# Optimization experiments

Hardware: AMD Instinct MI355X
Metric: run time of the kernel (lower is better)

Reference implementation:

```python
import jax, jax.numpy as jnp
import numpy as np

N, M, D, H = 2048, 32, 768, 512
TEMP, THRESH, EPS = 0.05, 1e-4, 1e-6


def setup_inputs() -> dict:
    key = jax.random.key(0)
    ks = jax.random.split(key, 7)
    q = jax.random.normal(ks[0], (D,), dtype=jnp.float32)
    X = jax.random.normal(ks[1], (N, D), dtype=jnp.float32)
    C_init = jax.random.normal(ks[2], (M, D), dtype=jnp.float32)
    # nn.Linear default init: U(-1/sqrt(fan_in), 1/sqrt(fan_in))
    s1 = 1.0 / np.sqrt(5 * D)
    W1 = jax.random.uniform(ks[3], (5 * D, H), jnp.float32, -s1, s1)
    b1 = jax.random.uniform(ks[4], (H,), jnp.float32, -s1, s1)
    s2 = 1.0 / np.sqrt(H)
    W2 = jax.random.uniform(ks[5], (H, 1), jnp.float32, -s2, s2)
    b2 = jax.random.uniform(ks[6], (1,), jnp.float32, -s2, s2)
    return {"q": q, "X": X, "C_init": C_init, "W1": W1, "b1": b1, "W2": W2, "b2": b2}


def _learned_dist(q, x, y, W1, b1, W2, b2):
    # pairwise features: for each (i,j): [x_i, y_j, |x_i-y_j|, |x_i-q|, |y_j-q|]
    n, m, d = x.shape[0], y.shape[0], x.shape[1]
    xb = jnp.broadcast_to(x[:, None, :], (n, m, d))
    yb = jnp.broadcast_to(y[None, :, :], (n, m, d))
    feat = jnp.concatenate(
        [xb, yb, jnp.abs(xb - yb), jnp.abs(xb - q), jnp.abs(yb - q)], axis=-1
    )  # (n, m, 5d)
    h = jax.nn.relu(jnp.einsum("nmf,fh->nmh", feat, W1) + b1)
    return jax.nn.sigmoid(jnp.einsum("nmh,ho->nmo", h, W2)[..., 0] + b2[0])  # (n, m)


def reference(q, X, C_init, W1, b1, W2, b2):
    d = -_learned_dist(q, X, C_init, W1, b1, W2, b2)          # (N, M)
    a = jax.nn.softmax(d / TEMP, axis=1)                       # (N, M)
    a_sum = jnp.sum(a, axis=0) + EPS                           # (M,)
    C_new = (a.T @ X) / a_sum[:, None]                         # (M, D)
    # Torch loop always recomputes with C_init, so it runs at most once and
    # returns C_new iff the initial diff exceeds the threshold, else C_init.
    diff = jnp.sum(jnp.abs(C_new - C_init))                    # L1 norm
    C_final = jnp.where(diff > THRESH, C_new, C_init)
    return (C_final, a)
```

## Files before the change

kernel.cpp:

```cpp
#include <hip/hip_runtime.h>
#include <hip/hip_fp16.h>
#include <math.h>

#define NN 2048
#define MM 32
#define DD 768
#define HH 512
#define KT 24
#define WBLK ((size_t)KT * 16384)
constexpr float TEMP = 0.05f;
constexpr float THRESH = 1e-4f;
constexpr float EPS = 1e-6f;

typedef _Float16 halfx8 __attribute__((ext_vector_type(8)));
typedef float floatx4 __attribute__((ext_vector_type(4)));

__device__ __forceinline__ halfx8 habs8(halfx8 a, halfx8 b) {
    halfx8 d = a - b;
    union { halfx8 h; unsigned int u[4]; } x;
    x.h = d;
    #pragma unroll
    for (int e = 0; e < 4; ++e) x.u[e] &= 0x7FFF7FFFu;
    return x.h;
}

__global__ __launch_bounds__(256) void prep_kernel(
    const float* __restrict__ X, const float* __restrict__ W1,
    _Float16* __restrict__ Xf, _Float16* __restrict__ Wf)
{
    __shared__ float Wt[32 * 512];
    const int t = threadIdx.x;
    if (blockIdx.x < 192) {
        #pragma unroll
        for (int p = 0; p < 4; ++p) {
            int u = blockIdx.x * 1024 + p * 256 + t;
            int it = u / 1536;
            int rem = u - it * 1536;
            int kt = rem >> 6;
            int lane = rem & 63;
            int row = it * 16 + (lane & 15);
            int kb = kt * 32 + (lane >> 4) * 8;
            const float* xp = X + (size_t)row * DD + kb;
            float4 xa = *(const float4*)xp;
            float4 xb = *(const float4*)(xp + 4);
            halfx8 v;
            v[0] = (_Float16)xa.x; v[1] = (_Float16)xa.y;
            v[2] = (_Float16)xa.z; v[3] = (_Float16)xa.w;
            v[4] = (_Float16)xb.x; v[5] = (_Float16)xb.y;
            v[6] = (_Float16)xb.z; v[7] = (_Float16)xb.w;
            *(halfx8*)(Xf + (size_t)u * 8) = v;
        }
    } else {
        const int b = blockIdx.x - 192;
        const int wb = b / 24;
        const int kt = b % 24;
        const int rowbase = wb * 768;
        #pragma unroll
        for (int rep = 0; rep < 16; ++rep) {
            int idx = rep * 256 + t;
            int row = idx >> 7;
            int c4 = (idx & 127) * 4;
            *(float4*)&Wt[row * 512 + c4] =
                *(const float4*)(W1 + (size_t)(rowbase + kt * 32 + row) * HH + c4);
        }
        __syncthreads();
        #pragma unroll
        for (int g = 0; g < 8; ++g) {
            halfx8 v;
            #pragma unroll
            for (int jj = 0; jj < 8; ++jj) {
                int o = t * 64 + g * 8 + jj;
                int nt = o >> 9;
                int l  = (o >> 3) & 63;
                int j  = o & 7;
                int k  = ((l >> 4) << 3) + j;
                int n  = nt * 16 + (l & 15);
                v[jj] = (_Float16)Wt[k * 512 + n];
            }
            *(halfx8*)(Wf + (size_t)wb * WBLK + (size_t)kt * 16384 + t * 64 + g * 8) = v;
        }
    }
}

__global__ __launch_bounds__(512, 2) void build_AB_kernel(
    const float* __restrict__ q, const float* __restrict__ C_init,
    const _Float16* __restrict__ Xf, const _Float16* __restrict__ Wf,
    const float* __restrict__ b1,
    _Float16* __restrict__ Arowh, float* __restrict__ Brow)
{
    __shared__ __align__(16) char smem[67584];
    const int t = threadIdx.x;
    const int lane = t & 63;
    const int wv = t >> 6;
    const int q4 = lane >> 4;
    const int l16 = lane & 15;

    if (blockIdx.x < 256) {
        _Float16* qh = (_Float16*)smem;
        const int hs = blockIdx.x & 3;
        const int by = blockIdx.x >> 2;
        const int nt = hs * 8 + wv;

        for (int d = t; d < DD; d += 512) qh[d] = (_Float16)q[d];
        __syncthreads();

        const _Float16* ap0 = Xf + ((size_t)((by * 2 + 0) * 24) * 64 + lane) * 8;
        const _Float16* ap1 = Xf + ((size_t)((by * 2 + 1) * 24) * 64 + lane) * 8;
        const _Float16* bpA = Wf + (size_t)nt * 512 + (size_t)lane * 8;
        const _Float16* bpD = Wf + 3 * WBLK + (size_t)nt * 512 + (size_t)lane * 8;

        floatx4 acc[2];
        acc[0] = (floatx4)0.f; acc[1] = (floatx4)0.f;

        halfx8 Afc[2], Bac, Bdc, Afn[2], Ban, Bdn;
        Afc[0] = *(const halfx8*)ap0;
        Afc[1] = *(const halfx8*)ap1;
        Bac = *(const halfx8*)bpA;
        Bdc = *(const halfx8*)bpD;

        for (int kt = 0; kt < KT; ++kt) {
            if (kt < KT - 1) {
                Afn[0] = *(const halfx8*)(ap0 + (kt + 1) * 512);
                Afn[1] = *(const halfx8*)(ap1 + (kt + 1) * 512);
                Ban = *(const halfx8*)(bpA + (size_t)(kt + 1) * 16384);
                Bdn = *(const halfx8*)(bpD + (size_t)(kt + 1) * 16384);
            }
            halfx8 qf = *(halfx8*)&qh[kt * 32 + q4 * 8];
            #pragma unroll
            for (int rt = 0; rt < 2; ++rt) {
                halfx8 Zd = habs8(Afc[rt], qf);
                acc[rt] = __builtin_amdgcn_mfma_f32_16x16x32_f16(Afc[rt], Bac, acc[rt], 0, 0, 0);
                acc[rt] = __builtin_amdgcn_mfma_f32_16x16x32_f16(Zd, Bdc, acc[rt], 0, 0, 0);
            }
            Afc[0] = Afn[0]; Afc[1] = Afn[1]; Bac = Ban; Bdc = Bdn;
        }
        #pragma unroll
        for (int rt = 0; rt < 2; ++rt)
            #pragma unroll
            for (int reg = 0; reg < 4; ++reg) {
                int i = by * 32 + rt * 16 + q4 * 4 + reg;
                int h = nt * 16 + l16;
                Arowh[(size_t)i * HH + h] = (_Float16)acc[rt][reg];
            }
    } else {
        _Float16* yh = (_Float16*)smem;
        _Float16* qh = yh + 32 * 776;
        floatx4* Bred = (floatx4*)(smem + (32 * 776 + DD) * 2);
        const int nt = blockIdx.x - 256;

        for (int r = 0; r < 32; ++r)
            for (int d = t; d < DD; d += 512)
                yh[r * 776 + d] = (_Float16)C_init[(size_t)r * DD + d];
        for (int d = t; d < DD; d += 512) qh[d] = (_Float16)q[d];
        __syncthreads();

        const _Float16* Wb = Wf + 1 * WBLK;
        const _Float16* We = Wf + 4 * WBLK;

        floatx4 acc[2];
        acc[0] = (floatx4)0.f; acc[1] = (floatx4)0.f;

        #pragma unroll
        for (int r = 0; r < 3; ++r) {
            int kt = wv + r * 8;
            halfx8 qf = *(halfx8*)&qh[kt * 32 + q4 * 8];
            size_t wo = (size_t)kt * 16384 + (size_t)nt * 512 + (size_t)lane * 8;
            halfx8 Bb = *(const halfx8*)(Wb + wo);
            halfx8 Be = *(const halfx8*)(We + wo);
            #pragma unroll
            for (int rt = 0; rt < 2; ++rt) {
                halfx8 Ab = *(halfx8*)&yh[(rt * 16 + l16) * 776 + kt * 32 + q4 * 8];
                halfx8 Ze = habs8(Ab, qf);
                acc[rt] = __builtin_amdgcn_mfma_f32_16x16x32_f16(Ab, Bb, acc[rt], 0, 0, 0);
                acc[rt] = __builtin_amdgcn_mfma_f32_16x16x32_f16(Ze, Be, acc[rt], 0, 0, 0);
            }
        }
        Bred[(wv * 2 + 0) * 64 + lane] = acc[0];
        Bred[(wv * 2 + 1) * 64 + lane] = acc[1];
        __syncthreads();
        if (wv < 2) {
            int rt = wv;
            floatx4 s = Bred[rt * 64 + lane];
            #pragma unroll
            for (int w = 1; w < 8; ++w) s += Bred[(w * 2 + rt) * 64 + lane];
            #pragma unroll
            for (int reg = 0; reg < 4; ++reg) {
                int j = rt * 16 + q4 * 4 + reg;
                int h = nt * 16 + l16;
                Brow[(size_t)j * HH + h] = s[reg] + b1[h];
            }
        }
    }
}

__global__ __launch_bounds__(512, 4) void pairwise_kernel(
    const _Float16* __restrict__ Xf, const _Float16* __restrict__ Wf,
    const float* __restrict__ Y,
    const _Float16* __restrict__ Arowh, const float* __restrict__ Brow,
    const float* __restrict__ W2, float* __restrict__ Spart)
{
    __shared__ _Float16 yh[2 * DD];
    __shared__ float Sred[2][4][64];
    const int t = threadIdx.x;
    const int lane = t & 63;
    const int wv = t >> 6;
    const int wr = wv >> 2;
    const int cq = wv & 3;
    const int q4 = lane >> 4;
    const int l16 = lane & 15;
    const int i0 = blockIdx.x * 64;
    const int hs = blockIdx.y & 1;
    const int j0 = (blockIdx.y >> 1) * 2;

    for (int d = t; d < DD; d += 512) {
        yh[d]      = (_Float16)Y[(size_t)j0 * DD + d];
        yh[DD + d] = (_Float16)Y[(size_t)(j0 + 1) * DD + d];
    }
    __syncthreads();

    const _Float16* Wc = Wf + 2 * WBLK;
    const _Float16* ap0 = Xf + ((size_t)((blockIdx.x * 4 + wr * 2 + 0) * 24) * 64 + lane) * 8;
    const _Float16* ap1 = Xf + ((size_t)((blockIdx.x * 4 + wr * 2 + 1) * 24) * 64 + lane) * 8;
    const _Float16* bp = Wc + (size_t)(hs * 16 + cq * 4) * 512 + (size_t)lane * 8;

    floatx4 acc[2][2][4];
    #pragma unroll
    for (int jj = 0; jj < 2; ++jj)
        #pragma unroll
        for (int rt = 0; rt < 2; ++rt)
            #pragma unroll
            for (int ct = 0; ct < 4; ++ct) acc[jj][rt][ct] = (floatx4)0.f;

    for (int kt = 0; kt < KT; ++kt) {
        halfx8 Af[2], Bf[4], hv[2];
        Af[0] = *(const halfx8*)(ap0 + kt * 512);
        Af[1] = *(const halfx8*)(ap1 + kt * 512);
        #pragma unroll
        for (int ct = 0; ct < 4; ++ct)
            Bf[ct] = *(const halfx8*)(bp + (size_t)kt * 16384 + ct * 512);
        hv[0] = *(halfx8*)&yh[kt * 32 + q4 * 8];
        hv[1] = *(halfx8*)&yh[DD + kt * 32 + q4 * 8];
        #pragma unroll
        for (int jj = 0; jj < 2; ++jj)
            #pragma unroll
            for (int rt = 0; rt < 2; ++rt) {
                halfx8 Zf = habs8(Af[rt], hv[jj]);
                #pragma unroll
                for (int ct = 0; ct < 4; ++ct)
                    acc[jj][rt][ct] = __builtin_amdgcn_mfma_f32_16x16x32_f16(
                        Zf, Bf[ct], acc[jj][rt][ct], 0, 0, 0);
            }
    }

    float w2v[4], bv[2][4];
    #pragma unroll
    for (int ct = 0; ct < 4; ++ct) {
        int h = hs * 256 + cq * 64 + ct * 16 + l16;
        w2v[ct] = W2[h];
        bv[0][ct] = Brow[(size_t)j0 * HH + h];
        bv[1][ct] = Brow[(size_t)(j0 + 1) * HH + h];
    }
    #pragma unroll
    for (int rt = 0; rt < 2; ++rt)
        #pragma unroll
        for (int reg = 0; reg < 4; ++reg) {
            int row = wr * 32 + rt * 16 + q4 * 4 + reg;
            const _Float16* ap = Arowh + (size_t)(i0 + row) * HH + hs * 256 + cq * 64 + l16;
            float av[4];
            #pragma unroll
            for (int ct = 0; ct < 4; ++ct) av[ct] = (float)ap[ct * 16];
            #pragma unroll
            for (int jj = 0; jj < 2; ++jj) {
                float s = 0.f;
                #pragma unroll
                for (int ct = 0; ct < 4; ++ct) {
                    float pre = acc[jj][rt][ct][reg] + av[ct] + bv[jj][ct];
                    s = fmaf(fmaxf(pre, 0.f), w2v[ct], s);
                }
                s += __shfl_xor(s, 1, 64);
                s += __shfl_xor(s, 2, 64);
                s += __shfl_xor(s, 4, 64);
                s += __shfl_xor(s, 8, 64);
                if (l16 == 0) Sred[jj][cq][row] = s;
            }
        }
    __syncthreads();
    if (t < 128) {
        int row = t & 63, jj = t >> 6;
        float s = Sred[jj][0][row] + Sred[jj][1][row] + Sred[jj][2][row] + Sred[jj][3][row];
        Spart[((size_t)hs * NN + (i0 + row)) * MM + j0 + jj] = s;
    }
}

__global__ __launch_bounds__(256) void cnew_sm_kernel(
    const float* __restrict__ Spart, const float* __restrict__ b2,
    const float* __restrict__ X,
    float* __restrict__ a_out, float* __restrict__ Cpart,
    float* __restrict__ Apart)
{
    __shared__ float a_s[64][36];
    const int t = threadIdx.x;
    const int dc = blockIdx.x;
    const int ic = blockIdx.y;
    const int ibase = ic * 64;
    const float b2v = b2[0];

    {
        const int j = t & 31, r = t >> 5;
        #pragma unroll
        for (int rb = 0; rb < 8; ++rb) {
            int il = rb * 8 + r;
            int i = ibase + il;
            float s = Spart[(size_t)i * MM + j] + Spart[(size_t)(NN + i) * MM + j];
            float sig = 1.f / (1.f + expf(-(s + b2v)));
            float l = -sig * (1.0f / TEMP);
            float m = l;
            #pragma unroll
            for (int off = 16; off >= 1; off >>= 1) m = fmaxf(m, __shfl_xor(m, off, 32));
            float e = expf(l - m);
            float sum = e;
            #pragma unroll
            for (int off = 16; off >= 1; off >>= 1) sum += __shfl_xor(sum, off, 32);
            a_s[il][j] = e / sum;
        }
    }
    __syncthreads();
    if (dc == 0) {
        #pragma unroll
        for (int p = 0; p < 8; ++p) {
            int k = p * 256 + t;
            a_out[(size_t)(ibase + (k >> 5)) * MM + (k & 31)] = a_s[k >> 5][k & 31];
        }
    }
    const int dl = t & 63, jg = t >> 6;
    const int d = dc * 64 + dl;
    float acc[8] = {};
    float asum[8] = {};
    #pragma unroll 4
    for (int ii = 0; ii < 64; ++ii) {
        float xv = X[(size_t)(ibase + ii) * DD + d];
        float4 a0 = *(float4*)&a_s[ii][jg * 8];
        float4 a1 = *(float4*)&a_s[ii][jg * 8 + 4];
        acc[0] = fmaf(a0.x, xv, acc[0]); asum[0] += a0.x;
        acc[1] = fmaf(a0.y, xv, acc[1]); asum[1] += a0.y;
        acc[2] = fmaf(a0.z, xv, acc[2]); asum[2] += a0.z;
        acc[3] = fmaf(a0.w, xv, acc[3]); asum[3] += a0.w;
        acc[4] = fmaf(a1.x, xv, acc[4]); asum[4] += a1.x;
        acc[5] = fmaf(a1.y, xv, acc[5]); asum[5] += a1.y;
        acc[6] = fmaf(a1.z, xv, acc[6]); asum[6] += a1.z;
        acc[7] = fmaf(a1.w, xv, acc[7]); asum[7] += a1.w;
    }
    #pragma unroll
    for (int jj = 0; jj < 8; ++jj)
        Cpart[((size_t)ic * MM + jg * 8 + jj) * DD + d] = acc[jj];
    if (dc == 0 && dl == 0)
        #pragma unroll
        for (int jj = 0; jj < 8; ++jj)
            Apart[ic * MM + jg * 8 + jj] = asum[jj];
}

__global__ __launch_bounds__(256) void merge_kernel(
    const float* __restrict__ Cpart, const float* __restrict__ Apart,
    const float* __restrict__ C_init, float* __restrict__ C_new,
    float* __restrict__ Dpart)
{
    __shared__ float wred[4];
    const int dc = blockIdx.x;
    const int j = blockIdx.y;
    const int t = threadIdx.x;
    const int d = dc * 256 + t;
    float asum = 0.f;
    #pragma unroll
    for (int ic = 0; ic < 32; ++ic) asum += Apart[ic * MM + j];
    const float inv = 1.f / (asum + EPS);
    float s = 0.f;
    #pragma unroll
    for (int ic = 0; ic < 32; ++ic)
        s += Cpart[((size_t)ic * MM + j) * DD + d];
    float c = s * inv;
    C_new[(size_t)j * DD + d] = c;
    float ad = fabsf(c - C_init[(size_t)j * DD + d]);
    #pragma unroll
    for (int off = 32; off >= 1; off >>= 1) ad += __shfl_xor(ad, off, 64);
    if ((t & 63) == 0) wred[t >> 6] = ad;
    __syncthreads();
    if (t == 0) Dpart[j * 3 + dc] = wred[0] + wred[1] + wred[2] + wred[3];
}

__global__ __launch_bounds__(256) void select_kernel(
    const float* __restrict__ C_new, const float* __restrict__ C_init,
    const float* __restrict__ Dpart, float* __restrict__ out)
{
    __shared__ float ds[96];
    const int t = threadIdx.x;
    if (t < 96) ds[t] = Dpart[t];
    __syncthreads();
    float dv = 0.f;
    #pragma unroll
    for (int p = 0; p < 96; ++p) dv += ds[p];
    const int k = blockIdx.x * 256 + t;
    out[k] = (dv > THRESH) ? C_new[k] : C_init[k];
}

extern "C" void kernel_launch(void* const* d_in, const int* in_sizes, int n_in,
                              void* d_out, int out_size, void* d_ws, size_t ws_size,
                              hipStream_t stream)
{
    const float* q      = (const float*)d_in[0];
    const float* X      = (const float*)d_in[1];
    const float* C_init = (const float*)d_in[2];
    const float* W1     = (const float*)d_in[3];
    const float* b1     = (const float*)d_in[4];
    const float* W2     = (const float*)d_in[5];
    const float* b2     = (const float*)d_in[6];

    float* out_C = (float*)d_out;
    float* out_a = (float*)d_out + (size_t)MM * DD;

    float* ws = (float*)d_ws;
    _Float16* Wf    = (_Float16*)ws;
    _Float16* Xf    = (_Float16*)(ws + 983040);
    _Float16* Arowh = (_Float16*)(ws + 1769472);
    float* Brow  = ws + 2293760;
    float* Spart = ws + 2310144;
    float* Cpart = ws + 2441216;
    float* Apart = ws + 3227648;
    float* Dpart = ws + 3228672;
    float* Cn    = ws + 3228768;

    prep_kernel<<<312, 256, 0, stream>>>(X, W1, Xf, Wf);
    build_AB_kernel<<<288, 512, 0, stream>>>(q, C_init, Xf, Wf, b1, Arowh, Brow);
    pairwise_kernel<<<dim3(32, 32), 512, 0, stream>>>(Xf, Wf, C_init, Arowh, Brow, W2, Spart);
    cnew_sm_kernel<<<dim3(12, 32), 256, 0, stream>>>(Spart, b2, X, out_a, Cpart, Apart);
    merge_kernel<<<dim3(3, 32), 256, 0, stream>>>(Cpart, Apart, C_init, Cn, Dpart);
    select_kernel<<<96, 256, 0, stream>>>(Cn, C_init, Dpart, out_C);
}
```

Before: 182.7 us.

## Retile pairwise kernel to one centroid per block with async LDS-staged X

Each pairwise block now handles a single centroid j across the full hidden dimension, with each wave owning a 64-wide hidden slice and all 64 rows. X fragments are staged into shared memory through double-buffered global_load_lds, so one X chunk is reused by all eight waves instead of each wave loading its own from global memory. This removes the two-way hidden split and its partial-sum buffer, so the softmax kernel reads one S value per entry. In exchange each wave holds more accumulators, the kernel uses more LDS, and W1 reuse across two centroids per block is lost, which may hurt occupancy and raise weight traffic.

```diff
diff --git a/kernel.cpp b/kernel.cpp
--- a/kernel.cpp
+++ b/kernel.cpp
@@ -197,103 +197,110 @@
     const _Float16* __restrict__ Xf, const _Float16* __restrict__ Wf,
     const float* __restrict__ Y,
     const _Float16* __restrict__ Arowh, const float* __restrict__ Brow,
-    const float* __restrict__ W2, float* __restrict__ Spart)
-{
-    __shared__ _Float16 yh[2 * DD];
-    __shared__ float Sred[2][4][64];
+    const float* __restrict__ W2, float* __restrict__ S)
+{
+    __shared__ _Float16 XfL[2 * 24 * 512];
+    __shared__ _Float16 yh[DD];
+    __shared__ float Sred[8][64];
     const int t = threadIdx.x;
     const int lane = t & 63;
     const int wv = t >> 6;
-    const int wr = wv >> 2;
-    const int cq = wv & 3;
     const int q4 = lane >> 4;
     const int l16 = lane & 15;
     const int i0 = blockIdx.x * 64;
-    const int hs = blockIdx.y & 1;
-    const int j0 = (blockIdx.y >> 1) * 2;
-
-    for (int d = t; d < DD; d += 512) {
-        yh[d]      = (_Float16)Y[(size_t)j0 * DD + d];
-        yh[DD + d] = (_Float16)Y[(size_t)(j0 + 1) * DD + d];
-    }
+    const int j  = blockIdx.y;
+
+    for (int d = t; d < DD; d += 512) yh[d] = (_Float16)Y[(size_t)j * DD + d];
+
+    const _Float16* Wc = Wf + 2 * WBLK;
+    const _Float16* bp = Wc + (size_t)(wv * 4) * 512 + (size_t)lane * 8;
+
+    auto stage = [&](int c, int buf) {
+        #pragma unroll
+        for (int s = 0; s < 3; ++s) {
+            int p = wv * 3 + s;
+            int ktc = p >> 2, it = p & 3;
+            const _Float16* src = Xf
+                + ((size_t)((blockIdx.x * 4 + it) * 24 + c * 6 + ktc) * 64 + lane) * 8;
+            _Float16* dst = &XfL[(buf * 24 + p) * 512];
+            __builtin_amdgcn_global_load_lds(
+                (const __attribute__((address_space(1))) unsigned int*)(const void*)src,
+                (__attribute__((address_space(3))) unsigned int*)(void*)dst, 16, 0, 0);
+        }
+    };
+
+    floatx4 acc[4][4];
+    #pragma unroll
+    for (int rt = 0; rt < 4; ++rt)
+        #pragma unroll
+        for (int ct = 0; ct < 4; ++ct) acc[rt][ct] = (floatx4)0.f;
+
+    stage(0, 0);
     __syncthreads();
 
-    const _Float16* Wc = Wf + 2 * WBLK;
-    const _Float16* ap0 = Xf + ((size_t)((blockIdx.x * 4 + wr * 2 + 0) * 24) * 64 + lane) * 8;
-    const _Float16* ap1 = Xf + ((size_t)((blockIdx.x * 4 + wr * 2 + 1) * 24) * 64 + lane) * 8;
-    const _Float16* bp = Wc + (size_t)(hs * 16 + cq * 4) * 512 + (size_t)lane * 8;
-
-    floatx4 acc[2][2][4];
-    #pragma unroll
-    for (int jj = 0; jj < 2; ++jj)
-        #pragma unroll
-        for (int rt = 0; rt < 2; ++rt)
-            #pragma unroll
-            for (int ct = 0; ct < 4; ++ct) acc[jj][rt][ct] = (floatx4)0.f;
-
-    for (int kt = 0; kt < KT; ++kt) {
-        halfx8 Af[2], Bf[4], hv[2];
-        Af[0] = *(const halfx8*)(ap0 + kt * 512);
-        Af[1] = *(const halfx8*)(ap1 + kt * 512);
-        #pragma unroll
-        for (int ct = 0; ct < 4; ++ct)
-            Bf[ct] = *(const halfx8*)(bp + (size_t)kt * 16384 + ct * 512);
-        hv[0] = *(halfx8*)&yh[kt * 32 + q4 * 8];
-        hv[1] = *(halfx8*)&yh[DD + kt * 32 + q4 * 8];
-        #pragma unroll
-        for (int jj = 0; jj < 2; ++jj)
-            #pragma unroll
-            for (int rt = 0; rt < 2; ++rt) {
-                halfx8 Zf = habs8(Af[rt], hv[jj]);
+    for (int c = 0; c < 4; ++c) {
+        if (c < 3) stage(c + 1, (c + 1) & 1);
+        const int buf = c & 1;
+        #pragma unroll
+        for (int ktc = 0; ktc < 6; ++ktc) {
+            const int kt = c * 6 + ktc;
+            halfx8 Bf[4];
+            #pragma unroll
+            for (int ct = 0; ct < 4; ++ct)
+                Bf[ct] = *(const halfx8*)(bp + (size_t)kt * 16384 + ct * 512);
+            halfx8 hv = *(halfx8*)&yh[kt * 32 + q4 * 8];
+            halfx8 Zf[4];
+            #pragma unroll
+            for (int rt = 0; rt < 4; ++rt) {
+                halfx8 Af = *(halfx8*)&XfL[((buf * 24 + ktc * 4 + rt) * 64 + lane) * 8];
+                Zf[rt] = habs8(Af, hv);
+            }
+            #pragma unroll
+            for (int ct = 0; ct < 4; ++ct)
                 #pragma unroll
-                for (int ct = 0; ct < 4; ++ct)
-                    acc[jj][rt][ct] = __builtin_amdgcn_mfma_f32_16x16x32_f16(
-                        Zf, Bf[ct], acc[jj][rt][ct], 0, 0, 0);
-            }
-    }
-
-    float w2v[4], bv[2][4];
+                for (int rt = 0; rt < 4; ++rt)
+                    acc[rt][ct] = __builtin_amdgcn_mfma_f32_16x16x32_f16(
+                        Zf[rt], Bf[ct], acc[rt][ct], 0, 0, 0);
+        }
+        __syncthreads();
+    }
+
+    float w2v[4], bv[4];
     #pragma unroll
     for (int ct = 0; ct < 4; ++ct) {
-        int h = hs * 256 + cq * 64 + ct * 16 + l16;
+        int h = wv * 64 + ct * 16 + l16;
         w2v[ct] = W2[h];
-        bv[0][ct] = Brow[(size_t)j0 * HH + h];
-        bv[1][ct] = Brow[(size_t)(j0 + 1) * HH + h];
-    }
-    #pragma unroll
-    for (int rt = 0; rt < 2; ++rt)
+        bv[ct]  = Brow[(size_t)j * HH + h];
+    }
+    #pragma unroll
+    for (int rt = 0; rt < 4; ++rt)
         #pragma unroll
         for (int reg = 0; reg < 4; ++reg) {
-            int row = wr * 32 + rt * 16 + q4 * 4 + reg;
-            const _Float16* ap = Arowh + (size_t)(i0 + row) * HH + hs * 256 + cq * 64 + l16;
-            float av[4];
-            #pragma unroll
-            for (int ct = 0; ct < 4; ++ct) av[ct] = (float)ap[ct * 16];
-            #pragma unroll
-            for (int jj = 0; jj < 2; ++jj) {
-                float s = 0.f;
-                #pragma unroll
-                for (int ct = 0; ct < 4; ++ct) {
-                    float pre = acc[jj][rt][ct][reg] + av[ct] + bv[jj][ct];
-                    s = fmaf(fmaxf(pre, 0.f), w2v[ct], s);
-                }
-                s += __shfl_xor(s, 1, 64);
-                s += __shfl_xor(s, 2, 64);
-                s += __shfl_xor(s, 4, 64);
-                s += __shfl_xor(s, 8, 64);
-                if (l16 == 0) Sred[jj][cq][row] = s;
-            }
+            int row = rt * 16 + q4 * 4 + reg;
+            const _Float16* ap = Arowh + (size_t)(i0 + row) * HH + wv * 64 + l16;
+            float s = 0.f;
+            #pragma unroll
+            for (int ct = 0; ct < 4; ++ct) {
+                float pre = acc[rt][ct][reg] + (float)ap[ct * 16] + bv[ct];
+                s = fmaf(fmaxf(pre, 0.f), w2v[ct], s);
+            }
+            s += __shfl_xor(s, 1, 64);
+            s += __shfl_xor(s, 2, 64);
+            s += __shfl_xor(s, 4, 64);
+            s += __shfl_xor(s, 8, 64);
+            if (l16 == 0) Sred[wv][row] = s;
         }
     __syncthreads();
-    if (t < 128) {
-        int row = t & 63, jj = t >> 6;
-        float s = Sred[jj][0][row] + Sred[jj][1][row] + Sred[jj][2][row] + Sred[jj][3][row];
-        Spart[((size_t)hs * NN + (i0 + row)) * MM + j0 + jj] = s;
+    if (t < 64) {
+        float s = 0.f;
+        #pragma unroll
+        for (int w = 0; w < 8; ++w) s += Sred[w][t];
+        S[(size_t)(i0 + t) * MM + j] = s;
     }
 }
 
 __global__ __launch_bounds__(256) void cnew_sm_kernel(
-    const float* __restrict__ Spart, const float* __restrict__ b2,
+    const float* __restrict__ S, const float* __restrict__ b2,
     const float* __restrict__ X,
     float* __restrict__ a_out, float* __restrict__ Cpart,
     float* __restrict__ Apart)
@@ -311,7 +318,7 @@
         for (int rb = 0; rb < 8; ++rb) {
             int il = rb * 8 + r;
             int i = ibase + il;
-            float s = Spart[(size_t)i * MM + j] + Spart[(size_t)(NN + i) * MM + j];
+            float s = S[(size_t)i * MM + j];
             float sig = 1.f / (1.f + expf(-(s + b2v)));
             float l = -sig * (1.0f / TEMP);
             float m = l;
@@ -422,16 +429,16 @@
     _Float16* Xf    = (_Float16*)(ws + 983040);
     _Float16* Arowh = (_Float16*)(ws + 1769472);
     float* Brow  = ws + 2293760;
-    float* Spart = ws + 2310144;
-    float* Cpart = ws + 2441216;
-    float* Apart = ws + 3227648;
-    float* Dpart = ws + 3228672;
-    float* Cn    = ws + 3228768;
+    float* S     = ws + 2310144;
+    float* Cpart = ws + 2375680;
+    float* Apart = ws + 3162112;
+    float* Dpart = ws + 3163136;
+    float* Cn    = ws + 3163232;
 
     prep_kernel<<<312, 256, 0, stream>>>(X, W1, Xf, Wf);
     build_AB_kernel<<<288, 512, 0, stream>>>(q, C_init, Xf, Wf, b1, Arowh, Brow);
-    pairwise_kernel<<<dim3(32, 32), 512, 0, stream>>>(Xf, Wf, C_init, Arowh, Brow, W2, Spart);
-    cnew_sm_kernel<<<dim3(12, 32), 256, 0, stream>>>(Spart, b2, X, out_a, Cpart, Apart);
+    pairwise_kernel<<<dim3(32, 32), 512, 0, stream>>>(Xf, Wf, C_init, Arowh, Brow, W2, S);
+    cnew_sm_kernel<<<dim3(12, 32), 256, 0, stream>>>(S, b2, X, out_a, Cpart, Apart);
     merge_kernel<<<dim3(3, 32), 256, 0, stream>>>(Cpart, Apart, C_init, Cn, Dpart);
     select_kernel<<<96, 256, 0, stream>>>(Cn, C_init, Dpart, out_C);
 }
```

New measurement: 190.4 us. +4.2%, slower.
